# Optimization experiments

Measured on AMD Instinct MI355X. Metric: run time of the kernel, lower is better.

The kernel has to match this reference:

```python
import jax, jax.numpy as jnp
import numpy as np

D_MODEL = 1024
N_HEADS = 16
D_K = D_MODEL // N_HEADS
TEMP = 0.01
THRESH = 0.019
NEG_INF = -1e9


def setup_inputs() -> dict:
    key = jax.random.key(0)
    ks = jax.random.split(key, 10)
    B, S = 4, 1024
    # xavier_uniform gain=1 for square [D,D]: limit = sqrt(6/(D+D))
    lim_w = float(np.sqrt(6.0 / (D_MODEL + D_MODEL)))
    # nn.Linear default bias init: U(-1/sqrt(fan_in), 1/sqrt(fan_in))
    lim_b = float(1.0 / np.sqrt(D_MODEL))
    return {
        "user_ID": jax.random.randint(ks[0], (B,), 0, 100000),
        "Q": jax.random.normal(ks[1], (B, S, D_MODEL), jnp.float32),
        "K": jax.random.normal(ks[2], (B, S, D_MODEL), jnp.float32),
        "V": jax.random.normal(ks[3], (B, S, D_MODEL), jnp.float32),
        "Wq": jax.random.uniform(ks[4], (D_MODEL, D_MODEL), jnp.float32, -lim_w, lim_w),
        "bq": jax.random.uniform(ks[5], (D_MODEL,), jnp.float32, -lim_b, lim_b),
        "Wk": jax.random.uniform(ks[6], (D_MODEL, D_MODEL), jnp.float32, -lim_w, lim_w),
        "bk": jax.random.uniform(ks[7], (D_MODEL,), jnp.float32, -lim_b, lim_b),
        "Wv": jax.random.uniform(ks[8], (D_MODEL, D_MODEL), jnp.float32, -lim_w, lim_w),
        "bv": jax.random.uniform(ks[9], (D_MODEL,), jnp.float32, -lim_b, lim_b),
    }


def _split_heads(x):
    B, S, _ = x.shape
    return x.reshape(B, S, N_HEADS, D_K).transpose(0, 2, 1, 3)  # [B,H,S,Dk]


def reference(user_ID, Q, K, V, Wq, bq, Wk, bk, Wv, bv):
    # nn.Linear: y = x @ W.T + b
    q = _split_heads(Q @ Wq.T + bq)
    k = _split_heads(K @ Wk.T + bk)
    v = _split_heads(V @ Wv.T + bv)
    scores = jnp.einsum("bhqd,bhkd->bhqk", q, k) / jnp.sqrt(jnp.float32(D_K))
    # temperature-sharpened softmax used only to build the sparse mask
    attn_sharp = jax.nn.softmax(scores / TEMP, axis=-1)
    mask_sparse = attn_sharp < THRESH
    scores = jnp.where(mask_sparse, jnp.float32(NEG_INF), scores)
    attn = jax.nn.softmax(scores, axis=-1)
    ctx = jnp.einsum("bhqk,bhkd->bhqd", attn, v)
    B, H, S, Dk = ctx.shape
    return ctx.transpose(0, 2, 1, 3).reshape(B, S, H * Dk)
```

## Files before the change

kernel.cpp:

```cpp
#include <hip/hip_runtime.h>

constexpr int D = 1024;
constexpr int S = 1024;
constexpr int NB = 4;
constexpr int NH = 16;
constexpr int DK = 64;
constexpr float THRESH = 0.019f;
constexpr int ROWS = 8;
constexpr int SSP = 1056;

typedef __attribute__((ext_vector_type(8))) short bf16x8;
typedef __attribute__((ext_vector_type(4))) float f32x4;

__device__ __forceinline__ float wave_max(float v) {
#pragma unroll
    for (int off = 32; off >= 1; off >>= 1)
        v = fmaxf(v, __shfl_xor(v, off, 64));
    return v;
}
__device__ __forceinline__ float wave_sum(float v) {
#pragma unroll
    for (int off = 32; off >= 1; off >>= 1)
        v += __shfl_xor(v, off, 64);
    return v;
}

__device__ __forceinline__ int cvtpk(float lo, float hi) {
    int r;
    asm("v_cvt_pk_bf16_f32 %0, %1, %2" : "=v"(r) : "v"(lo), "v"(hi));
    return r;
}
__device__ __forceinline__ bf16x8 pack_bf8(float4 a, float4 b) {
    union { int i[4]; bf16x8 v; } u;
    u.i[0] = cvtpk(a.x, a.y);
    u.i[1] = cvtpk(a.z, a.w);
    u.i[2] = cvtpk(b.x, b.y);
    u.i[3] = cvtpk(b.z, b.w);
    return u.v;
}

__global__ __launch_bounds__(256) void proj_kernel(
    const float* __restrict__ Qi, const float* __restrict__ Ki, const float* __restrict__ Vi,
    const float* __restrict__ Wq, const float* __restrict__ bq,
    const float* __restrict__ Wk, const float* __restrict__ bk,
    const float* __restrict__ Wv, const float* __restrict__ bv,
    float* __restrict__ qo, float* __restrict__ ko, float* __restrict__ vo)
{
    const int pz = blockIdx.z;
    const float* __restrict__ X    = (pz == 0) ? Qi : (pz == 1) ? Ki : Vi;
    const float* __restrict__ W    = (pz == 0) ? Wq : (pz == 1) ? Wk : Wv;
    const float* __restrict__ bias = (pz == 0) ? bq : (pz == 1) ? bk : bv;
    float* __restrict__ out        = (pz == 0) ? qo : (pz == 1) ? ko : vo;

    __shared__ __align__(16) float Xs[2][16][132];
    __shared__ __align__(16) float Ws[2][16][132];

    const int t  = threadIdx.x;
    const int tx = t & 15;
    const int ty = t >> 4;
    const int m0 = blockIdx.y * 128;
    const int n0 = blockIdx.x * 128;
    const int lr = t >> 1;
    const int lc = (t & 1) << 3;

    const float* __restrict__ Xp = X + (size_t)(m0 + lr) * D + lc;
    const float* __restrict__ Wp = W + (size_t)(n0 + lr) * D + lc;

    float4 xa = *(const float4*)(Xp + 0);
    float4 xb = *(const float4*)(Xp + 4);
    float4 wa = *(const float4*)(Wp + 0);
    float4 wb = *(const float4*)(Wp + 4);
    Xs[0][lc + 0][lr] = xa.x; Xs[0][lc + 1][lr] = xa.y; Xs[0][lc + 2][lr] = xa.z; Xs[0][lc + 3][lr] = xa.w;
    Xs[0][lc + 4][lr] = xb.x; Xs[0][lc + 5][lr] = xb.y; Xs[0][lc + 6][lr] = xb.z; Xs[0][lc + 7][lr] = xb.w;
    Ws[0][lc + 0][lr] = wa.x; Ws[0][lc + 1][lr] = wa.y; Ws[0][lc + 2][lr] = wa.z; Ws[0][lc + 3][lr] = wa.w;
    Ws[0][lc + 4][lr] = wb.x; Ws[0][lc + 5][lr] = wb.y; Ws[0][lc + 6][lr] = wb.z; Ws[0][lc + 7][lr] = wb.w;
    __syncthreads();

    float acc[8][8] = {};
    int buf = 0;

    for (int k0 = 0; k0 < D; k0 += 16) {
        const bool more = (k0 + 16) < D;
        if (more) {
            xa = *(const float4*)(Xp + k0 + 16);
            xb = *(const float4*)(Xp + k0 + 20);
            wa = *(const float4*)(Wp + k0 + 16);
            wb = *(const float4*)(Wp + k0 + 20);
        }
#pragma unroll
        for (int kk = 0; kk < 16; ++kk) {
            float4 a0 = *(const float4*)&Xs[buf][kk][(ty << 2)];
            float4 a1 = *(const float4*)&Xs[buf][kk][64 + (ty << 2)];
            float4 b0 = *(const float4*)&Ws[buf][kk][(tx << 2)];
            float4 b1 = *(const float4*)&Ws[buf][kk][64 + (tx << 2)];
            float av[8]  = {a0.x, a0.y, a0.z, a0.w, a1.x, a1.y, a1.z, a1.w};
            float bv8[8] = {b0.x, b0.y, b0.z, b0.w, b1.x, b1.y, b1.z, b1.w};
#pragma unroll
            for (int i = 0; i < 8; ++i)
#pragma unroll
                for (int j = 0; j < 8; ++j)
                    acc[i][j] += av[i] * bv8[j];
        }
        if (more) {
            const int nb = buf ^ 1;
            Xs[nb][lc + 0][lr] = xa.x; Xs[nb][lc + 1][lr] = xa.y; Xs[nb][lc + 2][lr] = xa.z; Xs[nb][lc + 3][lr] = xa.w;
            Xs[nb][lc + 4][lr] = xb.x; Xs[nb][lc + 5][lr] = xb.y; Xs[nb][lc + 6][lr] = xb.z; Xs[nb][lc + 7][lr] = xb.w;
            Ws[nb][lc + 0][lr] = wa.x; Ws[nb][lc + 1][lr] = wa.y; Ws[nb][lc + 2][lr] = wa.z; Ws[nb][lc + 3][lr] = wa.w;
            Ws[nb][lc + 4][lr] = wb.x; Ws[nb][lc + 5][lr] = wb.y; Ws[nb][lc + 6][lr] = wb.z; Ws[nb][lc + 7][lr] = wb.w;
            __syncthreads();
            buf = nb;
        }
    }

    const int bb2 = m0 >> 10;
    if (pz == 1) {
        const int s_base = (m0 & 1023) + (ty << 2);
#pragma unroll
        for (int g = 0; g < 2; ++g) {
            const int hh = (n0 >> 6) + g;
#pragma unroll
            for (int jj = 0; jj < 4; ++jj) {
                const int d = (tx << 2) + jj;
                const int j = (g << 2) + jj;
                const float bj = bias[n0 + (g << 6) + d];
                float* op = &out[(((size_t)bb2 * NH + hh) * DK + d) * S];
                *(float4*)(op + s_base) =
                    make_float4(acc[0][j] + bj, acc[1][j] + bj, acc[2][j] + bj, acc[3][j] + bj);
                *(float4*)(op + s_base + 64) =
                    make_float4(acc[4][j] + bj, acc[5][j] + bj, acc[6][j] + bj, acc[7][j] + bj);
            }
        }
    } else {
        float bj[8];
#pragma unroll
        for (int j = 0; j < 8; ++j)
            bj[j] = bias[n0 + ((j >> 2) << 6) + (tx << 2) + (j & 3)];
#pragma unroll
        for (int i = 0; i < 8; ++i) {
            const int sr = (m0 & 1023) + ((i >> 2) << 6) + (ty << 2) + (i & 3);
#pragma unroll
            for (int g = 0; g < 2; ++g) {
                const int hh = (n0 >> 6) + g;
                float* op = &out[(((size_t)bb2 * NH + hh) * S + sr) * DK + (tx << 2)];
                *(float4*)op = make_float4(acc[i][(g << 2) + 0] + bj[(g << 2) + 0],
                                           acc[i][(g << 2) + 1] + bj[(g << 2) + 1],
                                           acc[i][(g << 2) + 2] + bj[(g << 2) + 2],
                                           acc[i][(g << 2) + 3] + bj[(g << 2) + 3]);
            }
        }
    }
}

__global__ __launch_bounds__(256) void attn_kernel(
    const float* __restrict__ qw, const float* __restrict__ kw,
    const float* __restrict__ vw, float* __restrict__ out)
{
    __shared__ __align__(16) float ss[ROWS][SSP];
    __shared__ __align__(16) float qT[DK][ROWS];
    __shared__ float rowinv[ROWS];

    const int t    = threadIdx.x;
    const int lane = t & 63;
    const int w    = t >> 6;

    const int L   = blockIdx.x + (S / ROWS) * (blockIdx.y + NH * blockIdx.z);
    const int swz = (L & 7) * ((S / ROWS) * NH * NB / 8) + (L >> 3);
    const int qx  = swz & (S / ROWS - 1);
    const int h   = (swz >> 7) & (NH - 1);
    const int b   = swz >> 11;

    const size_t base = ((size_t)b * NH + h) * S * DK;
    const float* __restrict__ qp = qw + base;
    const float* __restrict__ kp = kw + base;
    const float* __restrict__ vp = vw + base;
    const int q0 = qx * ROWS;

#pragma unroll
    for (int p = 0; p < 2; ++p) {
        int e = t + 256 * p;
        int d = e >> 3, r = e & 7;
        qT[d][r] = qp[(size_t)(q0 + r) * DK + d] * 0.125f;
    }
    __syncthreads();

    float accf[ROWS][4] = {};
    const float* __restrict__ kTb = kp + 4 * t;

    float4 kbuf[4];
#pragma unroll
    for (int d = 0; d < 4; ++d)
        kbuf[d] = *(const float4*)&kTb[(size_t)d * S];

#pragma unroll
    for (int d0 = 0; d0 < DK; d0 += 4) {
        float4 kc[4] = {kbuf[0], kbuf[1], kbuf[2], kbuf[3]};
        if (d0 < DK - 4) {
#pragma unroll
            for (int d = 0; d < 4; ++d)
                kbuf[d] = *(const float4*)&kTb[(size_t)(d0 + 4 + d) * S];
        }
#pragma unroll
        for (int dd = 0; dd < 4; ++dd) {
            const int d = d0 + dd;
            float4 qa = *(const float4*)&qT[d][0];
            float4 qb = *(const float4*)&qT[d][4];
            float qr[8] = {qa.x, qa.y, qa.z, qa.w, qb.x, qb.y, qb.z, qb.w};
            float k4[4] = {kc[dd].x, kc[dd].y, kc[dd].z, kc[dd].w};
#pragma unroll
            for (int r = 0; r < ROWS; ++r)
#pragma unroll
                for (int i = 0; i < 4; ++i)
                    accf[r][i] += qr[r] * k4[i];
        }
    }
#pragma unroll
    for (int r = 0; r < ROWS; ++r)
        *(float4*)&ss[r][4 * t] = make_float4(accf[r][0], accf[r][1], accf[r][2], accf[r][3]);
    __syncthreads();

    for (int rr = w; rr < ROWS; rr += 4) {
        float mx = -3.4e38f;
#pragma unroll
        for (int p = 0; p < S / 64; ++p)
            mx = fmaxf(mx, ss[rr][lane + 64 * p]);
        mx = wave_max(mx);

        float zs = 0.f;
#pragma unroll
        for (int p = 0; p < S / 64; ++p)
            zs += __expf(100.f * (ss[rr][lane + 64 * p] - mx));
        zs = wave_sum(zs);

        const bool any = !((1.0f / zs) < THRESH);

        float z2 = 0.f;
#pragma unroll
        for (int p = 0; p < S / 64; ++p) {
            float x = ss[rr][lane + 64 * p];
            float e = __expf(100.f * (x - mx));
            bool keep = !((e / zs) < THRESH);
            float e2 = any ? (keep ? __expf(x - mx) : 0.f) : 1.f;
            z2 += e2;
            ss[rr][lane + 64 * p] = e2;
        }
        z2 = wave_sum(z2);
        if (lane == 0) rowinv[rr] = 1.0f / z2;
    }
    __syncthreads();

    {
        const int cr = lane & 15;
        const int gq = lane >> 4;
        const float* __restrict__ vB = vp + (size_t)(gq * 8) * DK + (w * 16 + cr);
        const float* __restrict__ arow = &ss[lane & 7][gq * 8];

        float bnx[8];
#pragma unroll
        for (int jj = 0; jj < 8; ++jj) bnx[jj] = vB[(size_t)jj * DK];

        f32x4 acc4 = {0.f, 0.f, 0.f, 0.f};
#pragma unroll 4
        for (int ks = 0; ks < 32; ++ks) {
            float bcur[8];
#pragma unroll
            for (int jj = 0; jj < 8; ++jj) bcur[jj] = bnx[jj];
            if (ks < 31) {
#pragma unroll
                for (int jj = 0; jj < 8; ++jj)
                    bnx[jj] = vB[(size_t)((ks + 1) * 32 + jj) * DK];
            }
            float4 a0 = *(const float4*)&arow[ks * 32];
            float4 a1 = *(const float4*)&arow[ks * 32 + 4];
            bf16x8 af = pack_bf8(a0, a1);
            bf16x8 bf = pack_bf8(make_float4(bcur[0], bcur[1], bcur[2], bcur[3]),
                                 make_float4(bcur[4], bcur[5], bcur[6], bcur[7]));
            acc4 = __builtin_amdgcn_mfma_f32_16x16x32_bf16(af, bf, acc4, 0, 0, 0);
        }

        if (gq < 2) {
            const int dcol = h * DK + w * 16 + cr;
#pragma unroll
            for (int reg = 0; reg < 4; ++reg) {
                const int r = gq * 4 + reg;
                out[((size_t)b * S + q0 + r) * D + dcol] = acc4[reg] * rowinv[r];
            }
        }
    }
}

extern "C" void kernel_launch(void* const* d_in, const int* in_sizes, int n_in,
                              void* d_out, int out_size, void* d_ws, size_t ws_size,
                              hipStream_t stream) {
    const float* Qi = (const float*)d_in[1];
    const float* Ki = (const float*)d_in[2];
    const float* Vi = (const float*)d_in[3];
    const float* Wq = (const float*)d_in[4];
    const float* bq = (const float*)d_in[5];
    const float* Wk = (const float*)d_in[6];
    const float* bk = (const float*)d_in[7];
    const float* Wv = (const float*)d_in[8];
    const float* bv = (const float*)d_in[9];
    float* outp = (float*)d_out;

    float* qws = (float*)d_ws;
    float* kws = qws + (size_t)NB * NH * S * DK;
    float* vws = kws + (size_t)NB * NH * S * DK;

    dim3 g1(D / 128, (NB * S) / 128, 3);
    proj_kernel<<<g1, 256, 0, stream>>>(Qi, Ki, Vi, Wq, bq, Wk, bk, Wv, bv, qws, kws, vws);

    dim3 g2(S / ROWS, NH, NB);
    attn_kernel<<<g2, 256, 0, stream>>>(qws, kws, vws, outp);
}
```

Measured before the change: 603.1 us.

## Split V projection into MFMA bf16 kernel writing transposed bf16 V

Moves the V projection out of the fp32 SIMT projection kernel into a new MFMA bf16 GEMM kernel that writes V as bf16, transposed to [B,H,DK,S]. The attention kernel then loads contiguous bf16x8 fragments of V directly, with a four-deep register ring, instead of gathering strided fp32 values and packing them. This is meant to cut V projection compute, halve V storage traffic and simplify the PV MFMA operand loads. The score buffer padding is also changed. The trade-off is an extra kernel launch and bf16 rounding of V at the projection stage, and the new GEMM reads operands straight from global memory without LDS reuse.

```diff
diff --git a/kernel.cpp b/kernel.cpp
--- a/kernel.cpp
+++ b/kernel.cpp
@@ -7,7 +7,7 @@
 constexpr int DK = 64;
 constexpr float THRESH = 0.019f;
 constexpr int ROWS = 8;
-constexpr int SSP = 1056;
+constexpr int SSP = 1044;
 
 typedef __attribute__((ext_vector_type(8))) short bf16x8;
 typedef __attribute__((ext_vector_type(4))) float f32x4;
@@ -40,17 +40,16 @@
 }
 
 __global__ __launch_bounds__(256) void proj_kernel(
-    const float* __restrict__ Qi, const float* __restrict__ Ki, const float* __restrict__ Vi,
+    const float* __restrict__ Qi, const float* __restrict__ Ki,
     const float* __restrict__ Wq, const float* __restrict__ bq,
     const float* __restrict__ Wk, const float* __restrict__ bk,
-    const float* __restrict__ Wv, const float* __restrict__ bv,
-    float* __restrict__ qo, float* __restrict__ ko, float* __restrict__ vo)
+    float* __restrict__ qo, float* __restrict__ ko)
 {
     const int pz = blockIdx.z;
-    const float* __restrict__ X    = (pz == 0) ? Qi : (pz == 1) ? Ki : Vi;
-    const float* __restrict__ W    = (pz == 0) ? Wq : (pz == 1) ? Wk : Wv;
-    const float* __restrict__ bias = (pz == 0) ? bq : (pz == 1) ? bk : bv;
-    float* __restrict__ out        = (pz == 0) ? qo : (pz == 1) ? ko : vo;
+    const float* __restrict__ X    = (pz == 0) ? Qi : Ki;
+    const float* __restrict__ W    = (pz == 0) ? Wq : Wk;
+    const float* __restrict__ bias = (pz == 0) ? bq : bk;
+    float* __restrict__ out        = (pz == 0) ? qo : ko;
 
     __shared__ __align__(16) float Xs[2][16][132];
     __shared__ __align__(16) float Ws[2][16][132];
@@ -151,9 +150,76 @@
     }
 }
 
+__global__ __launch_bounds__(256) void vproj_kernel(
+    const float* __restrict__ Vi, const float* __restrict__ Wv,
+    const float* __restrict__ bv, short* __restrict__ vo)
+{
+    const int t    = threadIdx.x;
+    const int lane = t & 63;
+    const int w    = t >> 6;
+    const int cr   = lane & 15;
+    const int gq   = lane >> 4;
+    const int d0   = blockIdx.x * 64;
+    const int sg0  = blockIdx.y * 64 + w * 16;
+
+    const float* __restrict__ Ap = Vi + (size_t)(sg0 + cr) * D + gq * 8;
+    const float* __restrict__ Bp = Wv + (size_t)(d0 + cr) * D + gq * 8;
+
+    f32x4 acc[4];
+#pragma unroll
+    for (int n = 0; n < 4; ++n) acc[n] = (f32x4){0.f, 0.f, 0.f, 0.f};
+
+    float4 a0c = *(const float4*)(Ap + 0);
+    float4 a1c = *(const float4*)(Ap + 4);
+    float4 b0c[4], b1c[4];
+#pragma unroll
+    for (int n = 0; n < 4; ++n) {
+        b0c[n] = *(const float4*)(Bp + (size_t)n * 16 * D + 0);
+        b1c[n] = *(const float4*)(Bp + (size_t)n * 16 * D + 4);
+    }
+
+    for (int k0 = 0; k0 < D; k0 += 32) {
+        const bool more = (k0 + 32) < D;
+        float4 a0n, a1n, b0n[4], b1n[4];
+        if (more) {
+            a0n = *(const float4*)(Ap + k0 + 32);
+            a1n = *(const float4*)(Ap + k0 + 36);
+#pragma unroll
+            for (int n = 0; n < 4; ++n) {
+                b0n[n] = *(const float4*)(Bp + (size_t)n * 16 * D + k0 + 32);
+                b1n[n] = *(const float4*)(Bp + (size_t)n * 16 * D + k0 + 36);
+            }
+        }
+        bf16x8 af = pack_bf8(a0c, a1c);
+#pragma unroll
+        for (int n = 0; n < 4; ++n)
+            acc[n] = __builtin_amdgcn_mfma_f32_16x16x32_bf16(
+                af, pack_bf8(b0c[n], b1c[n]), acc[n], 0, 0, 0);
+        if (more) {
+            a0c = a0n; a1c = a1n;
+#pragma unroll
+            for (int n = 0; n < 4; ++n) { b0c[n] = b0n[n]; b1c[n] = b1n[n]; }
+        }
+    }
+
+    const int sg = sg0 + gq * 4;
+    const int bb = sg >> 10;
+    const int sb = sg & 1023;
+#pragma unroll
+    for (int n = 0; n < 4; ++n) {
+        const int dg = d0 + n * 16 + cr;
+        const float bj = bv[dg];
+        const int hh = dg >> 6, dk = dg & 63;
+        const int p0 = cvtpk(acc[n][0] + bj, acc[n][1] + bj);
+        const int p1 = cvtpk(acc[n][2] + bj, acc[n][3] + bj);
+        short* op = vo + (((size_t)bb * NH + hh) * DK + dk) * S + sb;
+        *(int2*)op = make_int2(p0, p1);
+    }
+}
+
 __global__ __launch_bounds__(256) void attn_kernel(
     const float* __restrict__ qw, const float* __restrict__ kw,
-    const float* __restrict__ vw, float* __restrict__ out)
+    const short* __restrict__ vw, float* __restrict__ out)
 {
     __shared__ __align__(16) float ss[ROWS][SSP];
     __shared__ __align__(16) float qT[DK][ROWS];
@@ -172,7 +238,7 @@
     const size_t base = ((size_t)b * NH + h) * S * DK;
     const float* __restrict__ qp = qw + base;
     const float* __restrict__ kp = kw + base;
-    const float* __restrict__ vp = vw + base;
+    const short* __restrict__ vp = vw + base;
     const int q0 = qx * ROWS;
 
 #pragma unroll
@@ -251,30 +317,24 @@
     {
         const int cr = lane & 15;
         const int gq = lane >> 4;
-        const float* __restrict__ vB = vp + (size_t)(gq * 8) * DK + (w * 16 + cr);
+        const short* __restrict__ vTp = vp + (size_t)(w * 16 + cr) * S;
         const float* __restrict__ arow = &ss[lane & 7][gq * 8];
 
-        float bnx[8];
-#pragma unroll
-        for (int jj = 0; jj < 8; ++jj) bnx[jj] = vB[(size_t)jj * DK];
+        bf16x8 bring[4];
+#pragma unroll
+        for (int i = 0; i < 4; ++i)
+            bring[i] = *(const bf16x8*)&vTp[i * 32 + gq * 8];
 
         f32x4 acc4 = {0.f, 0.f, 0.f, 0.f};
-#pragma unroll 4
+#pragma unroll
         for (int ks = 0; ks < 32; ++ks) {
-            float bcur[8];
-#pragma unroll
-            for (int jj = 0; jj < 8; ++jj) bcur[jj] = bnx[jj];
-            if (ks < 31) {
-#pragma unroll
-                for (int jj = 0; jj < 8; ++jj)
-                    bnx[jj] = vB[(size_t)((ks + 1) * 32 + jj) * DK];
-            }
+            bf16x8 bcur = bring[ks & 3];
+            if (ks + 4 < 32)
+                bring[ks & 3] = *(const bf16x8*)&vTp[(ks + 4) * 32 + gq * 8];
             float4 a0 = *(const float4*)&arow[ks * 32];
             float4 a1 = *(const float4*)&arow[ks * 32 + 4];
             bf16x8 af = pack_bf8(a0, a1);
-            bf16x8 bf = pack_bf8(make_float4(bcur[0], bcur[1], bcur[2], bcur[3]),
-                                 make_float4(bcur[4], bcur[5], bcur[6], bcur[7]));
-            acc4 = __builtin_amdgcn_mfma_f32_16x16x32_bf16(af, bf, acc4, 0, 0, 0);
+            acc4 = __builtin_amdgcn_mfma_f32_16x16x32_bf16(af, bcur, acc4, 0, 0, 0);
         }
 
         if (gq < 2) {
@@ -304,10 +364,13 @@
 
     float* qws = (float*)d_ws;
     float* kws = qws + (size_t)NB * NH * S * DK;
-    float* vws = kws + (size_t)NB * NH * S * DK;
-
-    dim3 g1(D / 128, (NB * S) / 128, 3);
-    proj_kernel<<<g1, 256, 0, stream>>>(Qi, Ki, Vi, Wq, bq, Wk, bk, Wv, bv, qws, kws, vws);
+    short* vws = (short*)(kws + (size_t)NB * NH * S * DK);
+
+    dim3 gv(D / 64, (NB * S) / 64);
+    vproj_kernel<<<gv, 256, 0, stream>>>(Vi, Wv, bv, vws);
+
+    dim3 g1(D / 128, (NB * S) / 128, 2);
+    proj_kernel<<<g1, 256, 0, stream>>>(Qi, Ki, Wq, bq, Wk, bk, qws, kws);
 
     dim3 g2(S / ROWS, NH, NB);
     attn_kernel<<<g2, 256, 0, stream>>>(qws, kws, vws, outp);
```

Measured after the change: 706.9 us. 17.2% more time.

## Store V projection as transposed bf16 and prefetch V/K deeper in attention

Applied to the files above, without the earlier changes.

The projection kernel now writes V as bf16 in a transposed [d][s] layout, so the attention kernel loads ready-made bf16x8 MFMA operands with single 16-byte loads instead of eight strided fp32 loads plus conversion. V loads are issued before the softmax phase to hide their latency, and the K loads get two stages of double buffering issued before the Q staging. The LDS row padding is also changed. Rounding V to bf16 happens earlier, which matches the previous numerics since the values were already converted before the MFMA.

```diff
diff --git a/kernel.cpp b/kernel.cpp
--- a/kernel.cpp
+++ b/kernel.cpp
@@ -7,7 +7,7 @@
 constexpr int DK = 64;
 constexpr float THRESH = 0.019f;
 constexpr int ROWS = 8;
-constexpr int SSP = 1056;
+constexpr int SSP = 1044;
 
 typedef __attribute__((ext_vector_type(8))) short bf16x8;
 typedef __attribute__((ext_vector_type(4))) float f32x4;
@@ -44,13 +44,12 @@
     const float* __restrict__ Wq, const float* __restrict__ bq,
     const float* __restrict__ Wk, const float* __restrict__ bk,
     const float* __restrict__ Wv, const float* __restrict__ bv,
-    float* __restrict__ qo, float* __restrict__ ko, float* __restrict__ vo)
+    float* __restrict__ qo, float* __restrict__ ko, short* __restrict__ vo)
 {
     const int pz = blockIdx.z;
     const float* __restrict__ X    = (pz == 0) ? Qi : (pz == 1) ? Ki : Vi;
     const float* __restrict__ W    = (pz == 0) ? Wq : (pz == 1) ? Wk : Wv;
     const float* __restrict__ bias = (pz == 0) ? bq : (pz == 1) ? bk : bv;
-    float* __restrict__ out        = (pz == 0) ? qo : (pz == 1) ? ko : vo;
 
     __shared__ __align__(16) float Xs[2][16][132];
     __shared__ __align__(16) float Ws[2][16][132];
@@ -113,7 +112,7 @@
     }
 
     const int bb2 = m0 >> 10;
-    if (pz == 1) {
+    if (pz >= 1) {
         const int s_base = (m0 & 1023) + (ty << 2);
 #pragma unroll
         for (int g = 0; g < 2; ++g) {
@@ -123,11 +122,21 @@
                 const int d = (tx << 2) + jj;
                 const int j = (g << 2) + jj;
                 const float bj = bias[n0 + (g << 6) + d];
-                float* op = &out[(((size_t)bb2 * NH + hh) * DK + d) * S];
-                *(float4*)(op + s_base) =
-                    make_float4(acc[0][j] + bj, acc[1][j] + bj, acc[2][j] + bj, acc[3][j] + bj);
-                *(float4*)(op + s_base + 64) =
-                    make_float4(acc[4][j] + bj, acc[5][j] + bj, acc[6][j] + bj, acc[7][j] + bj);
+                if (pz == 1) {
+                    float* op = &ko[(((size_t)bb2 * NH + hh) * DK + d) * S];
+                    *(float4*)(op + s_base) =
+                        make_float4(acc[0][j] + bj, acc[1][j] + bj, acc[2][j] + bj, acc[3][j] + bj);
+                    *(float4*)(op + s_base + 64) =
+                        make_float4(acc[4][j] + bj, acc[5][j] + bj, acc[6][j] + bj, acc[7][j] + bj);
+                } else {
+                    short* op = &vo[(((size_t)bb2 * NH + hh) * DK + d) * S];
+                    *(int2*)(op + s_base) =
+                        make_int2(cvtpk(acc[0][j] + bj, acc[1][j] + bj),
+                                  cvtpk(acc[2][j] + bj, acc[3][j] + bj));
+                    *(int2*)(op + s_base + 64) =
+                        make_int2(cvtpk(acc[4][j] + bj, acc[5][j] + bj),
+                                  cvtpk(acc[6][j] + bj, acc[7][j] + bj));
+                }
             }
         }
     } else {
@@ -141,7 +150,7 @@
 #pragma unroll
             for (int g = 0; g < 2; ++g) {
                 const int hh = (n0 >> 6) + g;
-                float* op = &out[(((size_t)bb2 * NH + hh) * S + sr) * DK + (tx << 2)];
+                float* op = &qo[(((size_t)bb2 * NH + hh) * S + sr) * DK + (tx << 2)];
                 *(float4*)op = make_float4(acc[i][(g << 2) + 0] + bj[(g << 2) + 0],
                                            acc[i][(g << 2) + 1] + bj[(g << 2) + 1],
                                            acc[i][(g << 2) + 2] + bj[(g << 2) + 2],
@@ -153,7 +162,7 @@
 
 __global__ __launch_bounds__(256) void attn_kernel(
     const float* __restrict__ qw, const float* __restrict__ kw,
-    const float* __restrict__ vw, float* __restrict__ out)
+    const short* __restrict__ vw, float* __restrict__ out)
 {
     __shared__ __align__(16) float ss[ROWS][SSP];
     __shared__ __align__(16) float qT[DK][ROWS];
@@ -172,8 +181,15 @@
     const size_t base = ((size_t)b * NH + h) * S * DK;
     const float* __restrict__ qp = qw + base;
     const float* __restrict__ kp = kw + base;
-    const float* __restrict__ vp = vw + base;
+    const short* __restrict__ vp = vw + base;
     const int q0 = qx * ROWS;
+
+    const float* __restrict__ kTb = kp + 4 * t;
+    float4 kbuf[2][4];
+#pragma unroll
+    for (int d = 0; d < 4; ++d) kbuf[0][d] = *(const float4*)&kTb[(size_t)d * S];
+#pragma unroll
+    for (int d = 0; d < 4; ++d) kbuf[1][d] = *(const float4*)&kTb[(size_t)(4 + d) * S];
 
 #pragma unroll
     for (int p = 0; p < 2; ++p) {
@@ -184,24 +200,17 @@
     __syncthreads();
 
     float accf[ROWS][4] = {};
-    const float* __restrict__ kTb = kp + 4 * t;
-
-    float4 kbuf[4];
-#pragma unroll
-    for (int d = 0; d < 4; ++d)
-        kbuf[d] = *(const float4*)&kTb[(size_t)d * S];
-
-#pragma unroll
-    for (int d0 = 0; d0 < DK; d0 += 4) {
-        float4 kc[4] = {kbuf[0], kbuf[1], kbuf[2], kbuf[3]};
-        if (d0 < DK - 4) {
+#pragma unroll
+    for (int st = 0; st < 16; ++st) {
+        float4 kc[4] = {kbuf[st & 1][0], kbuf[st & 1][1], kbuf[st & 1][2], kbuf[st & 1][3]};
+        if (st < 14) {
 #pragma unroll
             for (int d = 0; d < 4; ++d)
-                kbuf[d] = *(const float4*)&kTb[(size_t)(d0 + 4 + d) * S];
+                kbuf[st & 1][d] = *(const float4*)&kTb[(size_t)((st + 2) * 4 + d) * S];
         }
 #pragma unroll
         for (int dd = 0; dd < 4; ++dd) {
-            const int d = d0 + dd;
+            const int d = st * 4 + dd;
             float4 qa = *(const float4*)&qT[d][0];
             float4 qb = *(const float4*)&qT[d][4];
             float qr[8] = {qa.x, qa.y, qa.z, qa.w, qb.x, qb.y, qb.z, qb.w};
@@ -217,6 +226,14 @@
     for (int r = 0; r < ROWS; ++r)
         *(float4*)&ss[r][4 * t] = make_float4(accf[r][0], accf[r][1], accf[r][2], accf[r][3]);
     __syncthreads();
+
+    const int cr = lane & 15;
+    const int gq = lane >> 4;
+    const short* __restrict__ vTp = vp + (size_t)(w * 16 + cr) * S;
+    bf16x8 bring[8];
+#pragma unroll
+    for (int i = 0; i < 8; ++i)
+        bring[i] = *(const bf16x8*)&vTp[i * 32 + gq * 8];
 
     for (int rr = w; rr < ROWS; rr += 4) {
         float mx = -3.4e38f;
@@ -249,32 +266,18 @@
     __syncthreads();
 
     {
-        const int cr = lane & 15;
-        const int gq = lane >> 4;
-        const float* __restrict__ vB = vp + (size_t)(gq * 8) * DK + (w * 16 + cr);
         const float* __restrict__ arow = &ss[lane & 7][gq * 8];
 
-        float bnx[8];
-#pragma unroll
-        for (int jj = 0; jj < 8; ++jj) bnx[jj] = vB[(size_t)jj * DK];
-
         f32x4 acc4 = {0.f, 0.f, 0.f, 0.f};
-#pragma unroll 4
+#pragma unroll
         for (int ks = 0; ks < 32; ++ks) {
-            float bcur[8];
-#pragma unroll
-            for (int jj = 0; jj < 8; ++jj) bcur[jj] = bnx[jj];
-            if (ks < 31) {
-#pragma unroll
-                for (int jj = 0; jj < 8; ++jj)
-                    bnx[jj] = vB[(size_t)((ks + 1) * 32 + jj) * DK];
-            }
+            bf16x8 bcur = bring[ks & 7];
+            if (ks + 8 < 32)
+                bring[ks & 7] = *(const bf16x8*)&vTp[(ks + 8) * 32 + gq * 8];
             float4 a0 = *(const float4*)&arow[ks * 32];
             float4 a1 = *(const float4*)&arow[ks * 32 + 4];
             bf16x8 af = pack_bf8(a0, a1);
-            bf16x8 bf = pack_bf8(make_float4(bcur[0], bcur[1], bcur[2], bcur[3]),
-                                 make_float4(bcur[4], bcur[5], bcur[6], bcur[7]));
-            acc4 = __builtin_amdgcn_mfma_f32_16x16x32_bf16(af, bf, acc4, 0, 0, 0);
+            acc4 = __builtin_amdgcn_mfma_f32_16x16x32_bf16(af, bcur, acc4, 0, 0, 0);
         }
 
         if (gq < 2) {
@@ -304,7 +307,7 @@
 
     float* qws = (float*)d_ws;
     float* kws = qws + (size_t)NB * NH * S * DK;
-    float* vws = kws + (size_t)NB * NH * S * DK;
+    short* vws = (short*)(kws + (size_t)NB * NH * S * DK);
 
     dim3 g1(D / 128, (NB * S) / 128, 3);
     proj_kernel<<<g1, 256, 0, stream>>>(Qi, Ki, Vi, Wq, bq, Wk, bk, Wv, bv, qws, kws, vws);
```

After: 623.6 us. +3.4%, slower.

## Compute V projection with bf16 MFMA in a separate kernel

Applied to the files above, without the earlier changes.

Moves the V projection out of the fp32 projection kernel into a new kernel that converts V and Wv tiles to bf16 in shared memory and multiplies them with 16x16x32 bf16 MFMA instructions. The original projection kernel now handles only Q and K. V carries no thresholded mask, so reduced precision there is intended to trade some accuracy for matrix-core throughput, while Q and K stay fp32 to keep the sparse-mask decisions exact. It adds an extra kernel launch and lower precision on the V values.

```diff
diff --git a/kernel.cpp b/kernel.cpp
--- a/kernel.cpp
+++ b/kernel.cpp
@@ -148,6 +148,66 @@
                                            acc[i][(g << 2) + 3] + bj[(g << 2) + 3]);
             }
         }
+    }
+}
+
+__global__ __launch_bounds__(256) void vproj_kernel(
+    const float* __restrict__ Vi, const float* __restrict__ Wv,
+    const float* __restrict__ bv, float* __restrict__ vo)
+{
+    __shared__ __align__(16) short Ah[64][40];
+    __shared__ __align__(16) short Bh[64][40];
+
+    const int t    = threadIdx.x;
+    const int lane = t & 63;
+    const int w    = t >> 6;
+    const int cr   = lane & 15;
+    const int gq   = lane >> 4;
+    const int m0   = blockIdx.y * 64;
+    const int n0   = blockIdx.x * 64;
+
+    const int ar = t >> 2, kq = t & 3;
+    const float* __restrict__ Ap = Vi + (size_t)(m0 + ar) * D + kq * 8;
+    const float* __restrict__ Bp = Wv + (size_t)(n0 + ar) * D + kq * 8;
+
+    float4 a0 = *(const float4*)(Ap + 0), a1 = *(const float4*)(Ap + 4);
+    float4 b0 = *(const float4*)(Bp + 0), b1 = *(const float4*)(Bp + 4);
+
+    f32x4 acc[4];
+#pragma unroll
+    for (int nj = 0; nj < 4; ++nj) acc[nj] = (f32x4){0.f, 0.f, 0.f, 0.f};
+
+    for (int ks = 0; ks < 32; ++ks) {
+        *(int4*)&Ah[ar][kq * 8] = make_int4(cvtpk(a0.x, a0.y), cvtpk(a0.z, a0.w),
+                                            cvtpk(a1.x, a1.y), cvtpk(a1.z, a1.w));
+        *(int4*)&Bh[ar][kq * 8] = make_int4(cvtpk(b0.x, b0.y), cvtpk(b0.z, b0.w),
+                                            cvtpk(b1.x, b1.y), cvtpk(b1.z, b1.w));
+        __syncthreads();
+        if (ks < 31) {
+            a0 = *(const float4*)(Ap + (ks + 1) * 32 + 0);
+            a1 = *(const float4*)(Ap + (ks + 1) * 32 + 4);
+            b0 = *(const float4*)(Bp + (ks + 1) * 32 + 0);
+            b1 = *(const float4*)(Bp + (ks + 1) * 32 + 4);
+        }
+        bf16x8 af = *(const bf16x8*)&Ah[16 * w + cr][gq * 8];
+#pragma unroll
+        for (int nj = 0; nj < 4; ++nj) {
+            bf16x8 bf = *(const bf16x8*)&Bh[16 * nj + cr][gq * 8];
+            acc[nj] = __builtin_amdgcn_mfma_f32_16x16x32_bf16(af, bf, acc[nj], 0, 0, 0);
+        }
+        __syncthreads();
+    }
+
+    const int bb = m0 >> 10;
+    const int s0 = (m0 & 1023) + 16 * w + 4 * gq;
+    const int hh = n0 >> 6;
+#pragma unroll
+    for (int nj = 0; nj < 4; ++nj) {
+        const int dk = 16 * nj + cr;
+        const float bj = bv[n0 + dk];
+#pragma unroll
+        for (int reg = 0; reg < 4; ++reg)
+            vo[(((size_t)bb * NH + hh) * S + s0 + reg) * DK + dk] = acc[nj][reg] + bj;
     }
 }
 
@@ -306,7 +366,10 @@
     float* kws = qws + (size_t)NB * NH * S * DK;
     float* vws = kws + (size_t)NB * NH * S * DK;
 
-    dim3 g1(D / 128, (NB * S) / 128, 3);
+    dim3 gv(D / 64, (NB * S) / 64);
+    vproj_kernel<<<gv, 256, 0, stream>>>(Vi, Wv, bv, vws);
+
+    dim3 g1(D / 128, (NB * S) / 128, 2);
     proj_kernel<<<g1, 256, 0, stream>>>(Qi, Ki, Vi, Wq, bq, Wk, bk, Wv, bv, qws, kws, vws);
 
     dim3 g2(S / ROWS, NH, NB);
```

Result: faster. 558.2 us (-7.4%).
